# Optimization experiments

Hardware: AMD Instinct MI355X
Metric: run time of the kernel (lower is better)

## Reference

```python
import jax, jax.numpy as jnp
import numpy as np


def _binarize_except_outliers(weight):
    # torch.mean / torch.std over the flattened weight; torch.std is unbiased (ddof=1)
    mean = jnp.mean(weight)
    std = jnp.std(weight, ddof=1)
    lower = mean - std
    upper = mean + std
    outliers = (weight < lower) | (weight > upper)
    # non-outliers -> sign(w) (STEBinary forward); outliers keep original fp values
    return jnp.where(outliers, weight, jnp.sign(weight))


def setup_inputs() -> dict:
    key = jax.random.key(0)
    k1, k2, k3 = jax.random.split(key, 3)
    B, S, D_IN, D_OUT = 8, 2048, 4096, 4096
    x = jax.random.normal(k1, (B, S, D_IN), dtype=jnp.float32)
    weight = jax.random.normal(k2, (D_OUT, D_IN), dtype=jnp.float32) * 0.02
    bias = jax.random.normal(k3, (D_OUT,), dtype=jnp.float32) * 0.02
    return {"x": x, "weight": weight, "bias": bias}


def reference(x, weight, bias):
    w_bin = _binarize_except_outliers(weight)  # [d_out, d_in]
    # F.linear: x @ w.T + b
    out = jnp.einsum("bsd,od->bso", x, w_bin) + bias
    return out
```

## Files before the change

### kernel.cpp

```cpp
#include <hip/hip_runtime.h>
#include <stdint.h>
#include <math.h>

typedef __attribute__((ext_vector_type(8))) short short8;
typedef __attribute__((ext_vector_type(4))) float f32x4;

typedef const __attribute__((address_space(1))) void* gas_ptr;
typedef __attribute__((address_space(3))) void* las_ptr;

__device__ __forceinline__ void gld_lds16(const void* g, void* l) {
    __builtin_amdgcn_global_load_lds((gas_ptr)g, (las_ptr)l, 16, 0, 0);
}

__device__ __forceinline__ unsigned short f32_to_bf16_rne(float f) {
    unsigned u = __builtin_bit_cast(unsigned, f);
    u += 0x7FFFu + ((u >> 16) & 1u);
    return (unsigned short)(u >> 16);
}

__global__ void stats_partial_kernel(const float* __restrict__ w, int n4, double* __restrict__ partials) {
    __shared__ double ssum[256];
    __shared__ double ssq[256];
    int t = threadIdx.x;
    long i = (long)blockIdx.x * blockDim.x + t;
    long stride = (long)gridDim.x * blockDim.x;
    double s = 0.0, q = 0.0;
    for (; i < n4; i += stride) {
        float4 v = ((const float4*)w)[i];
        s += (double)v.x + (double)v.y + (double)v.z + (double)v.w;
        q += (double)v.x * v.x + (double)v.y * v.y + (double)v.z * v.z + (double)v.w * v.w;
    }
    ssum[t] = s; ssq[t] = q;
    __syncthreads();
    for (int off = 128; off > 0; off >>= 1) {
        if (t < off) { ssum[t] += ssum[t + off]; ssq[t] += ssq[t + off]; }
        __syncthreads();
    }
    if (t == 0) {
        partials[2 * blockIdx.x]     = ssum[0];
        partials[2 * blockIdx.x + 1] = ssq[0];
    }
}

__global__ void stats_final_kernel(const double* __restrict__ partials, int nblocks, long n,
                                   float* __restrict__ bounds) {
    __shared__ double ssum[256];
    __shared__ double ssq[256];
    int t = threadIdx.x;
    double s = 0.0, q = 0.0;
    for (int i = t; i < nblocks; i += 256) {
        s += partials[2 * i];
        q += partials[2 * i + 1];
    }
    ssum[t] = s; ssq[t] = q;
    __syncthreads();
    for (int off = 128; off > 0; off >>= 1) {
        if (t < off) { ssum[t] += ssum[t + off]; ssq[t] += ssq[t + off]; }
        __syncthreads();
    }
    if (t == 0) {
        double sum = ssum[0], sumsq = ssq[0];
        double mean = sum / (double)n;
        double var = (sumsq - sum * sum / (double)n) / (double)(n - 1);
        double sd = sqrt(var);
        bounds[0] = (float)(mean - sd);
        bounds[1] = (float)(mean + sd);
    }
}

__global__ void binarize_w_kernel(const float* __restrict__ w, const float* __restrict__ bounds,
                                  unsigned short* __restrict__ wb, long n4) {
    float lo = bounds[0], hi = bounds[1];
    long i = (long)blockIdx.x * blockDim.x + threadIdx.x;
    if (i >= n4) return;
    float4 v = ((const float4*)w)[i];
    float r[4] = {v.x, v.y, v.z, v.w};
    ushort4 o;
    unsigned short ob[4];
#pragma unroll
    for (int j = 0; j < 4; j++) {
        float f = r[j];
        bool outlier = (f < lo) || (f > hi);
        float b = outlier ? f : (f > 0.f ? 1.f : (f < 0.f ? -1.f : 0.f));
        ob[j] = f32_to_bf16_rne(b);
    }
    o.x = ob[0]; o.y = ob[1]; o.z = ob[2]; o.w = ob[3];
    ((ushort4*)wb)[i] = o;
}

__global__ void convert_x_kernel(const float* __restrict__ x, unsigned short* __restrict__ xb, long n4) {
    long i = (long)blockIdx.x * blockDim.x + threadIdx.x;
    if (i >= n4) return;
    float4 v = ((const float4*)x)[i];
    ushort4 o;
    o.x = f32_to_bf16_rne(v.x);
    o.y = f32_to_bf16_rne(v.y);
    o.z = f32_to_bf16_rne(v.z);
    o.w = f32_to_bf16_rne(v.w);
    ((ushort4*)xb)[i] = o;
}

#define BM 128
#define BN 128
#define BK 64

__global__ __launch_bounds__(256) void gemm_bt_kernel(
    const unsigned short* __restrict__ A,
    const unsigned short* __restrict__ B,
    const float* __restrict__ bias,
    float* __restrict__ C,
    int M, int N, int K)
{
    __shared__ __align__(16) unsigned short As[BM * BK];
    __shared__ __align__(16) unsigned short Bs[BN * BK];

    const int t = threadIdx.x;
    const int wave = t >> 6;
    const int lane = t & 63;
    const int wr = wave >> 1;
    const int wc = wave & 1;
    const int lm = lane & 15;
    const int quad = lane >> 4;
    const int sw = lm & 7;

    const int tile_m = blockIdx.y * BM;
    const int tile_n = blockIdx.x * BN;

    f32x4 acc[4][4] = {};

    int row_[4], src_[4];
#pragma unroll
    for (int j = 0; j < 4; j++) {
        int c = j * 256 + t;
        int r = c >> 3, kc = c & 7;
        row_[j] = r;
        src_[j] = (kc ^ (r & 7)) * 8;
    }
    const int lds_base = wave * 512;

    const size_t Astripe = (size_t)tile_m * K;
    const size_t Bstripe = (size_t)tile_n * K;

    for (int kt = 0; kt < K; kt += BK) {
#pragma unroll
        for (int j = 0; j < 4; j++) {
            gld_lds16(A + Astripe + (size_t)row_[j] * K + kt + src_[j], &As[j * 2048 + lds_base]);
            gld_lds16(B + Bstripe + (size_t)row_[j] * K + kt + src_[j], &Bs[j * 2048 + lds_base]);
        }
        __syncthreads();

#pragma unroll
        for (int s = 0; s < 2; s++) {
            short8 af[4], bf[4];
#pragma unroll
            for (int i = 0; i < 4; i++) {
                int arow = wr * 64 + i * 16 + lm;
                int achunk = (s * 4 + quad) ^ sw;
                af[i] = *(const short8*)&As[arow * 64 + achunk * 8];
                int brow = wc * 64 + i * 16 + lm;
                bf[i] = *(const short8*)&Bs[brow * 64 + achunk * 8];
            }
#pragma unroll
            for (int i = 0; i < 4; i++)
#pragma unroll
                for (int j = 0; j < 4; j++)
                    acc[i][j] = __builtin_amdgcn_mfma_f32_16x16x32_bf16(af[i], bf[j], acc[i][j], 0, 0, 0);
        }
        __syncthreads();
    }

#pragma unroll
    for (int j = 0; j < 4; j++) {
        int col = tile_n + wc * 64 + j * 16 + lm;
        float bv = bias[col];
#pragma unroll
        for (int i = 0; i < 4; i++) {
            int row0 = tile_m + wr * 64 + i * 16 + quad * 4;
#pragma unroll
            for (int r = 0; r < 4; r++) {
                C[(size_t)(row0 + r) * N + col] = acc[i][j][r] + bv;
            }
        }
    }
}

__global__ void gemm_fallback_kernel(const float* __restrict__ A, const float* __restrict__ W,
                                     const float* __restrict__ bias, const float* __restrict__ bounds,
                                     float* __restrict__ C, int M, int N, int K) {
    __shared__ float as[16][16];
    __shared__ float wsm[16][17];
    int tx = threadIdx.x, ty = threadIdx.y;
    int row = blockIdx.y * 16 + ty;
    int col = blockIdx.x * 16 + tx;
    float lo = bounds[0], hi = bounds[1];
    float acc = 0.f;
    for (int k0 = 0; k0 < K; k0 += 16) {
        as[ty][tx] = A[(size_t)row * K + k0 + tx];
        float wv = W[(size_t)(blockIdx.x * 16 + ty) * K + k0 + tx];
        bool outlier = (wv < lo) || (wv > hi);
        wsm[ty][tx] = outlier ? wv : (wv > 0.f ? 1.f : (wv < 0.f ? -1.f : 0.f));
        __syncthreads();
#pragma unroll
        for (int k = 0; k < 16; k++) acc += as[ty][k] * wsm[tx][k];
        __syncthreads();
    }
    C[(size_t)row * N + col] = acc + bias[col];
}

extern "C" void kernel_launch(void* const* d_in, const int* in_sizes, int n_in,
                              void* d_out, int out_size, void* d_ws, size_t ws_size,
                              hipStream_t stream) {
    const float* x    = (const float*)d_in[0];
    const float* w    = (const float*)d_in[1];
    const float* bias = (const float*)d_in[2];
    float* out = (float*)d_out;

    const int  N  = in_sizes[2];
    const long wn = (long)in_sizes[1];
    const int  K  = (int)(wn / N);
    const long xn = (long)in_sizes[0];
    const int  M  = (int)(xn / K);

    char* ws = (char*)d_ws;
    float*  bounds   = (float*)ws;
    double* partials = (double*)(ws + 64);
    const size_t wb_off = 16512;
    unsigned short* wb = (unsigned short*)(ws + wb_off);
    const size_t xb_off = wb_off + (size_t)wn * 2;
    unsigned short* xb = (unsigned short*)(ws + xb_off);
    const size_t need_full = xb_off + (size_t)xn * 2;

    stats_partial_kernel<<<1024, 256, 0, stream>>>(w, (int)(wn / 4), partials);
    stats_final_kernel<<<1, 256, 0, stream>>>(partials, 1024, wn, bounds);

    if (ws_size >= need_full) {
        long wn4 = wn / 4, xn4 = xn / 4;
        binarize_w_kernel<<<(int)((wn4 + 255) / 256), 256, 0, stream>>>(w, bounds, wb, wn4);
        convert_x_kernel<<<(int)((xn4 + 255) / 256), 256, 0, stream>>>(x, xb, xn4);
        dim3 grid(N / BN, M / BM);
        gemm_bt_kernel<<<grid, 256, 0, stream>>>(xb, wb, bias, out, M, N, K);
    } else {
        dim3 grid(N / 16, M / 16), blk(16, 16);
        gemm_fallback_kernel<<<grid, blk, 0, stream>>>(x, w, bias, bounds, out, M, N, K);
    }
}
```

Baseline: 1.206 ms.

## Fuse weight/activation conversion kernels and add grouped tile ordering for GEMM

Merges the weight-binarize and x-to-bf16 kernels into one grid-stride kernel, which saves a launch. The GEMM grid becomes 1D and is remapped into 16x16 super-tiles so that concurrently running blocks share A and B stripes in L2. The stats partial grid is halved. The super-tile mapping adds some index arithmetic and relies on tile counts being multiples of 16, with a fallback ordering otherwise.

```diff
diff --git a/kernel.cpp b/kernel.cpp
--- a/kernel.cpp
+++ b/kernel.cpp
@@ -18,7 +18,7 @@
     return (unsigned short)(u >> 16);
 }
 
-__global__ void stats_partial_kernel(const float* __restrict__ w, int n4, double* __restrict__ partials) {
+__global__ void stats_partial_kernel(const float* __restrict__ w, long n4, double* __restrict__ partials) {
     __shared__ double ssum[256];
     __shared__ double ssq[256];
     int t = threadIdx.x;
@@ -68,36 +68,39 @@
     }
 }
 
-__global__ void binarize_w_kernel(const float* __restrict__ w, const float* __restrict__ bounds,
-                                  unsigned short* __restrict__ wb, long n4) {
-    float lo = bounds[0], hi = bounds[1];
+__global__ void fused_convert_kernel(const float* __restrict__ x, const float* __restrict__ w,
+                                     const float* __restrict__ bounds,
+                                     unsigned short* __restrict__ xb, unsigned short* __restrict__ wb,
+                                     long xn4, long wn4) {
+    const float lo = bounds[0], hi = bounds[1];
+    const long total = wn4 + xn4;
     long i = (long)blockIdx.x * blockDim.x + threadIdx.x;
-    if (i >= n4) return;
-    float4 v = ((const float4*)w)[i];
-    float r[4] = {v.x, v.y, v.z, v.w};
-    ushort4 o;
-    unsigned short ob[4];
-#pragma unroll
-    for (int j = 0; j < 4; j++) {
-        float f = r[j];
-        bool outlier = (f < lo) || (f > hi);
-        float b = outlier ? f : (f > 0.f ? 1.f : (f < 0.f ? -1.f : 0.f));
-        ob[j] = f32_to_bf16_rne(b);
-    }
-    o.x = ob[0]; o.y = ob[1]; o.z = ob[2]; o.w = ob[3];
-    ((ushort4*)wb)[i] = o;
-}
-
-__global__ void convert_x_kernel(const float* __restrict__ x, unsigned short* __restrict__ xb, long n4) {
-    long i = (long)blockIdx.x * blockDim.x + threadIdx.x;
-    if (i >= n4) return;
-    float4 v = ((const float4*)x)[i];
-    ushort4 o;
-    o.x = f32_to_bf16_rne(v.x);
-    o.y = f32_to_bf16_rne(v.y);
-    o.z = f32_to_bf16_rne(v.z);
-    o.w = f32_to_bf16_rne(v.w);
-    ((ushort4*)xb)[i] = o;
+    const long stride = (long)gridDim.x * blockDim.x;
+    for (; i < total; i += stride) {
+        if (i < wn4) {
+            float4 v = ((const float4*)w)[i];
+            float r[4] = {v.x, v.y, v.z, v.w};
+            unsigned short ob[4];
+#pragma unroll
+            for (int j = 0; j < 4; j++) {
+                float f = r[j];
+                bool outlier = (f < lo) || (f > hi);
+                float b = outlier ? f : (f > 0.f ? 1.f : (f < 0.f ? -1.f : 0.f));
+                ob[j] = f32_to_bf16_rne(b);
+            }
+            ushort4 o; o.x = ob[0]; o.y = ob[1]; o.z = ob[2]; o.w = ob[3];
+            ((ushort4*)wb)[i] = o;
+        } else {
+            long j = i - wn4;
+            float4 v = ((const float4*)x)[j];
+            ushort4 o;
+            o.x = f32_to_bf16_rne(v.x);
+            o.y = f32_to_bf16_rne(v.y);
+            o.z = f32_to_bf16_rne(v.z);
+            o.w = f32_to_bf16_rne(v.w);
+            ((ushort4*)xb)[j] = o;
+        }
+    }
 }
 
 #define BM 128
@@ -123,8 +126,20 @@
     const int quad = lane >> 4;
     const int sw = lm & 7;
 
-    const int tile_m = blockIdx.y * BM;
-    const int tile_n = blockIdx.x * BN;
+    const int grid_m = M / BM, grid_n = N / BN;
+    int tile_m, tile_n;
+    if ((grid_m & 15) == 0 && (grid_n & 15) == 0) {
+        int pid = blockIdx.x;
+        int within = pid & 255;
+        int st = pid >> 8;
+        int stm = grid_m >> 4;
+        int st_m = st % stm, st_n = st / stm;
+        tile_m = (st_m * 16 + (within >> 4)) * BM;
+        tile_n = (st_n * 16 + (within & 15)) * BN;
+    } else {
+        tile_m = (blockIdx.x / grid_n) * BM;
+        tile_n = (blockIdx.x % grid_n) * BN;
+    }
 
     f32x4 acc[4][4] = {};
 
@@ -230,17 +245,16 @@
     unsigned short* xb = (unsigned short*)(ws + xb_off);
     const size_t need_full = xb_off + (size_t)xn * 2;
 
-    stats_partial_kernel<<<1024, 256, 0, stream>>>(w, (int)(wn / 4), partials);
-    stats_final_kernel<<<1, 256, 0, stream>>>(partials, 1024, wn, bounds);
+    stats_partial_kernel<<<512, 256, 0, stream>>>(w, wn / 4, partials);
+    stats_final_kernel<<<1, 256, 0, stream>>>(partials, 512, wn, bounds);
 
     if (ws_size >= need_full) {
         long wn4 = wn / 4, xn4 = xn / 4;
-        binarize_w_kernel<<<(int)((wn4 + 255) / 256), 256, 0, stream>>>(w, bounds, wb, wn4);
-        convert_x_kernel<<<(int)((xn4 + 255) / 256), 256, 0, stream>>>(x, xb, xn4);
-        dim3 grid(N / BN, M / BM);
-        gemm_bt_kernel<<<grid, 256, 0, stream>>>(xb, wb, bias, out, M, N, K);
+        fused_convert_kernel<<<2048, 256, 0, stream>>>(x, w, bounds, xb, wb, xn4, wn4);
+        int nblocks = (M / BM) * (N / BN);
+        gemm_bt_kernel<<<nblocks, 256, 0, stream>>>(xb, wb, bias, out, M, N, K);
     } else {
         dim3 grid(N / 16, M / 16), blk(16, 16);
-        gemm_fallback_kernel<<<grid, blk, 0, stream>>>(x, w, bias, bounds, out, M, N, K);
-    }
-}
+        gemm_fallback_kernel<<<grid, blk, 0, stream>>>(x, w, bounds ? bias : bias, bounds, out, M, N, K);
+    }
+}
```

After: 1.209 ms. About the same (+0.3%).
